# Kernel optimization log

Measured on AMD Instinct MI355X. Metric: run time of the kernel, lower is better.

Reference implementation:

```python
import jax, jax.numpy as jnp
import numpy as np

N_NODES = 100000
N_EDGES = 1600000
NODE_DIM = 64
EDGE_DIM = 32
HIDDEN = 128
OUT_DIM = 64


def setup_inputs() -> dict:
    key = jax.random.key(0)
    ks = jax.random.split(key, 6)
    x = jax.random.normal(ks[0], (N_NODES, NODE_DIM), dtype=jnp.float32)
    edge_attr = jax.random.normal(ks[1], (N_EDGES, EDGE_DIM), dtype=jnp.float32)
    in_dim = 2 * NODE_DIM + EDGE_DIM  # 160
    W1 = jax.random.normal(ks[2], (in_dim, HIDDEN), dtype=jnp.float32) * (1.0 / np.sqrt(in_dim))
    b1 = jnp.zeros((HIDDEN,), dtype=jnp.float32)
    W2 = jax.random.normal(ks[3], (HIDDEN, OUT_DIM), dtype=jnp.float32) * (1.0 / np.sqrt(HIDDEN))
    b2 = jnp.zeros((OUT_DIM,), dtype=jnp.float32)
    edge_index = jax.random.randint(ks[4], (2, N_EDGES), 0, N_NODES, dtype=jnp.int64)
    return {"x": x, "edge_attr": edge_attr, "W1": W1, "b1": b1, "W2": W2, "b2": b2,
            "edge_index": edge_index}


def reference(x, edge_attr, W1, b1, W2, b2, edge_index):
    src, tgt = edge_index[0], edge_index[1]
    # gather source/target node features, concat with edge features: [E, 2*node_dim+edge_dim]
    merged = jnp.concatenate([x[src], x[tgt], edge_attr], axis=1)
    h = jax.nn.relu(merged @ W1 + b1)   # [E, HIDDEN]
    return h @ W2 + b2                  # [E, OUT_DIM]
```

## Files before the change

### kernel.cpp

```cpp
#include <hip/hip_runtime.h>

#define E_TOTAL 1600000
#define N_NODES 100000
#define ND 64
#define ED 32
#define IN_DIM 160
#define HID 128
#define OUTD 64

#define TM 128
#define H_STRIDE 136

typedef short v8s __attribute__((ext_vector_type(8)));
typedef float v4f __attribute__((ext_vector_type(4)));

__device__ __forceinline__ unsigned short f2bf(float f) {
    union { float f; unsigned u; } v; v.f = f;
    unsigned u = v.u;
    u += 0x7FFFu + ((u >> 16) & 1u);
    return (unsigned short)(u >> 16);
}

__device__ __forceinline__ v8s cvt8(float4 f0, float4 f1) {
    v8s r;
    r[0] = (short)f2bf(f0.x); r[1] = (short)f2bf(f0.y);
    r[2] = (short)f2bf(f0.z); r[3] = (short)f2bf(f0.w);
    r[4] = (short)f2bf(f1.x); r[5] = (short)f2bf(f1.y);
    r[6] = (short)f2bf(f1.z); r[7] = (short)f2bf(f1.w);
    return r;
}

__global__ void prep_x(const float* __restrict__ x, unsigned short* __restrict__ xbf) {
    int i = blockIdx.x * blockDim.x + threadIdx.x;
    if (i < N_NODES * ND) xbf[i] = f2bf(x[i]);
}

__global__ void prep_weights(const float* __restrict__ W1, const float* __restrict__ W2,
                             unsigned short* __restrict__ w1f, unsigned short* __restrict__ w2f) {
    int i = blockIdx.x * blockDim.x + threadIdx.x;
    if (i < IN_DIM * HID) {
        int t8 = i & 7, lane = (i >> 3) & 63, jk = i >> 9;
        int kk = jk >> 3, jt = jk & 7, cc = lane & 15, qq = lane >> 4;
        int n = jt * 16 + cc, k = kk * 32 + qq * 8 + t8;
        w1f[i] = f2bf(W1[k * HID + n]);
    } else if (i < IN_DIM * HID + HID * OUTD) {
        int u = i - IN_DIM * HID;
        int t8 = u & 7, lane = (u >> 3) & 63, jk = u >> 9;
        int kk = jk >> 2, jt = jk & 3, cc = lane & 15, qq = lane >> 4;
        int n = jt * 16 + cc, k = kk * 32 + qq * 8 + t8;
        w2f[u] = f2bf(W2[k * OUTD + n]);
    }
}

template<bool XBF>
__global__ __launch_bounds__(256, 4) void edge_mlp(
    const float* __restrict__ x, const unsigned short* __restrict__ xbf,
    const float* __restrict__ ea,
    const float* __restrict__ b1, const float* __restrict__ b2,
    const int* __restrict__ eidx,
    const unsigned short* __restrict__ w1f, const unsigned short* __restrict__ w2f,
    float* __restrict__ out)
{
    __shared__ unsigned short h[TM * H_STRIDE];

    const int tid = threadIdx.x, lane = tid & 63, w = tid >> 6;
    const int wr = w >> 1, wc = w & 1, c = lane & 15, q = lane >> 4;
    const int e0 = blockIdx.x * TM;

    int eRow[4], srcOff[4], tgtOff[4];
#pragma unroll
    for (int i = 0; i < 4; ++i) {
        eRow[i] = e0 + wr * 64 + i * 16 + c;
        srcOff[i] = eidx[eRow[i]] * ND;
        tgtOff[i] = eidx[E_TOTAL + eRow[i]] * ND;
    }

    v4f acc[4][4] = {};
#pragma unroll
    for (int kk = 0; kk < 5; ++kk) {
        v8s a[4];
#pragma unroll
        for (int i = 0; i < 4; ++i) {
            if (kk < 4) {
                const int off = (kk < 2 ? srcOff[i] : tgtOff[i]) + (kk & 1) * 32 + q * 8;
                if (XBF) {
                    a[i] = *(const v8s*)(xbf + off);
                } else {
                    const float4* p = (const float4*)(x + off);
                    a[i] = cvt8(p[0], p[1]);
                }
            } else {
                const float4* p = (const float4*)(ea + (long)eRow[i] * ED + q * 8);
                a[i] = cvt8(p[0], p[1]);
            }
        }
        v8s b[4];
#pragma unroll
        for (int j = 0; j < 4; ++j)
            b[j] = *(const v8s*)(w1f + ((kk * 8 + wc * 4 + j) * 64 + lane) * 8);
#pragma unroll
        for (int i = 0; i < 4; ++i)
#pragma unroll
            for (int j = 0; j < 4; ++j)
                acc[i][j] = __builtin_amdgcn_mfma_f32_16x16x32_bf16(a[i], b[j], acc[i][j], 0, 0, 0);
    }

#pragma unroll
    for (int j = 0; j < 4; ++j) {
        const float bias = b1[wc * 64 + j * 16 + c];
#pragma unroll
        for (int i = 0; i < 4; ++i) {
#pragma unroll
            for (int r = 0; r < 4; ++r) {
                float v = acc[i][j][r] + bias;
                v = v > 0.f ? v : 0.f;
                h[(wr * 64 + i * 16 + q * 4 + r) * H_STRIDE + wc * 64 + j * 16 + c] = f2bf(v);
            }
        }
    }
    __syncthreads();

    v4f acc2[4][2] = {};
#pragma unroll
    for (int kk = 0; kk < 4; ++kk) {
        v8s a[4];
#pragma unroll
        for (int i = 0; i < 4; ++i)
            a[i] = *(const v8s*)(h + (wr * 64 + i * 16 + c) * H_STRIDE + kk * 32 + q * 8);
        v8s b[2];
#pragma unroll
        for (int j = 0; j < 2; ++j)
            b[j] = *(const v8s*)(w2f + ((kk * 4 + wc * 2 + j) * 64 + lane) * 8);
#pragma unroll
        for (int i = 0; i < 4; ++i)
#pragma unroll
            for (int j = 0; j < 2; ++j)
                acc2[i][j] = __builtin_amdgcn_mfma_f32_16x16x32_bf16(a[i], b[j], acc2[i][j], 0, 0, 0);
    }

#pragma unroll
    for (int j = 0; j < 2; ++j) {
        const float bias = b2[wc * 32 + j * 16 + c];
#pragma unroll
        for (int i = 0; i < 4; ++i) {
#pragma unroll
            for (int r = 0; r < 4; ++r) {
                const long e = (long)e0 + wr * 64 + i * 16 + q * 4 + r;
                out[e * OUTD + wc * 32 + j * 16 + c] = acc2[i][j][r] + bias;
            }
        }
    }
}

extern "C" void kernel_launch(void* const* d_in, const int* in_sizes, int n_in,
                              void* d_out, int out_size, void* d_ws, size_t ws_size,
                              hipStream_t stream) {
    const float* x  = (const float*)d_in[0];
    const float* ea = (const float*)d_in[1];
    const float* W1 = (const float*)d_in[2];
    const float* b1 = (const float*)d_in[3];
    const float* W2 = (const float*)d_in[4];
    const float* b2 = (const float*)d_in[5];
    const int* eidx = (const int*)d_in[6];
    float* out = (float*)d_out;

    const size_t nx = (size_t)N_NODES * ND;
    const size_t need = (nx + IN_DIM * HID + HID * OUTD) * 2;
    const int nw = IN_DIM * HID + HID * OUTD;

    if (ws_size >= need) {
        unsigned short* xbf = (unsigned short*)d_ws;
        unsigned short* w1f = xbf + nx;
        unsigned short* w2f = w1f + IN_DIM * HID;
        prep_x<<<(int)((nx + 255) / 256), 256, 0, stream>>>(x, xbf);
        prep_weights<<<(nw + 255) / 256, 256, 0, stream>>>(W1, W2, w1f, w2f);
        edge_mlp<true><<<E_TOTAL / TM, 256, 0, stream>>>(x, xbf, ea, b1, b2, eidx, w1f, w2f, out);
    } else {
        unsigned short* w1f = (unsigned short*)d_ws;
        unsigned short* w2f = w1f + IN_DIM * HID;
        prep_weights<<<(nw + 255) / 256, 256, 0, stream>>>(W1, W2, w1f, w2f);
        edge_mlp<false><<<E_TOTAL / TM, 256, 0, stream>>>(x, nullptr, ea, b1, b2, eidx, w1f, w2f, out);
    }
}
```

Baseline: 734.0 us.

## Process two edge tiles per block with software prefetch of next tile's gathers

Each block now handles two 128-edge tiles. While the second GEMM of the first tile runs, the block prefetches the second tile's node-feature gathers and edge attributes into registers, so gather latency overlaps with MFMA work. Non-temporal loads and stores are used for the streamed edge attributes, indices and output to reduce cache pollution. Launch bounds drop from 4 to 3 blocks per SM to make room for the extra prefetch registers, which lowers occupancy and halves the grid size.

```diff
diff --git a/kernel.cpp b/kernel.cpp
--- a/kernel.cpp
+++ b/kernel.cpp
@@ -21,18 +21,19 @@
     return (unsigned short)(u >> 16);
 }
 
-__device__ __forceinline__ v8s cvt8(float4 f0, float4 f1) {
+__device__ __forceinline__ v8s cvt8v(v4f f0, v4f f1) {
     v8s r;
-    r[0] = (short)f2bf(f0.x); r[1] = (short)f2bf(f0.y);
-    r[2] = (short)f2bf(f0.z); r[3] = (short)f2bf(f0.w);
-    r[4] = (short)f2bf(f1.x); r[5] = (short)f2bf(f1.y);
-    r[6] = (short)f2bf(f1.z); r[7] = (short)f2bf(f1.w);
+#pragma unroll
+    for (int t = 0; t < 4; ++t) {
+        r[t]     = (short)f2bf(f0[t]);
+        r[t + 4] = (short)f2bf(f1[t]);
+    }
     return r;
 }
 
 __global__ void prep_x(const float* __restrict__ x, unsigned short* __restrict__ xbf) {
     int i = blockIdx.x * blockDim.x + threadIdx.x;
-    if (i < N_NODES * ND) xbf[i] = f2bf(x[i]);
+    if (i < N_NODES * ND) xbf[i] = f2bf(__builtin_nontemporal_load(x + i));
 }
 
 __global__ void prep_weights(const float* __restrict__ W1, const float* __restrict__ W2,
@@ -52,8 +53,118 @@
     }
 }
 
+template<bool XBF, bool PREFETCH>
+__device__ __forceinline__ void tile_body(
+    unsigned short* h,
+    const float* __restrict__ x, const unsigned short* __restrict__ xbf,
+    const float* __restrict__ ea,
+    const float* __restrict__ b1, const float* __restrict__ b2,
+    const unsigned short* __restrict__ w1f, const unsigned short* __restrict__ w2f,
+    float* __restrict__ out,
+    const int lane, const int wr, const int wc, const int c, const int q,
+    const int (&eRow)[4], const int (&srcOff)[4], const int (&tgtOff)[4],
+    v8s (&ax)[4][4], v4f (&eaf)[4][2],
+    const int (&eRowN)[4], const int (&srcOffN)[4], const int (&tgtOffN)[4],
+    v8s (&axN)[4][4], v4f (&eafN)[4][2])
+{
+    v4f acc[4][4] = {};
+#pragma unroll
+    for (int kk = 0; kk < 5; ++kk) {
+        v8s a[4];
+#pragma unroll
+        for (int i = 0; i < 4; ++i) {
+            if (kk < 4) {
+                if constexpr (XBF) {
+                    a[i] = ax[i][kk];
+                } else {
+                    const int off = (kk < 2 ? srcOff[i] : tgtOff[i]) + (kk & 1) * 32 + q * 8;
+                    const v4f* p = (const v4f*)(x + off);
+                    a[i] = cvt8v(p[0], p[1]);
+                }
+            } else {
+                a[i] = cvt8v(eaf[i][0], eaf[i][1]);
+            }
+        }
+        v8s b[4];
+#pragma unroll
+        for (int j = 0; j < 4; ++j)
+            b[j] = *(const v8s*)(w1f + ((kk * 8 + wc * 4 + j) * 64 + lane) * 8);
+#pragma unroll
+        for (int i = 0; i < 4; ++i)
+#pragma unroll
+            for (int j = 0; j < 4; ++j)
+                acc[i][j] = __builtin_amdgcn_mfma_f32_16x16x32_bf16(a[i], b[j], acc[i][j], 0, 0, 0);
+    }
+
+#pragma unroll
+    for (int j = 0; j < 4; ++j) {
+        const float bias = b1[wc * 64 + j * 16 + c];
+#pragma unroll
+        for (int i = 0; i < 4; ++i) {
+#pragma unroll
+            for (int r = 0; r < 4; ++r) {
+                float v = acc[i][j][r] + bias;
+                v = v > 0.f ? v : 0.f;
+                h[(wr * 64 + i * 16 + q * 4 + r) * H_STRIDE + wc * 64 + j * 16 + c] = f2bf(v);
+            }
+        }
+    }
+    __syncthreads();
+
+    if constexpr (PREFETCH && XBF) {
+#pragma unroll
+        for (int i = 0; i < 4; ++i) {
+            axN[i][0] = *(const v8s*)(xbf + srcOffN[i] + q * 8);
+            axN[i][1] = *(const v8s*)(xbf + srcOffN[i] + 32 + q * 8);
+            axN[i][2] = *(const v8s*)(xbf + tgtOffN[i] + q * 8);
+            axN[i][3] = *(const v8s*)(xbf + tgtOffN[i] + 32 + q * 8);
+        }
+    }
+
+    v4f acc2[4][2] = {};
+#pragma unroll
+    for (int kk = 0; kk < 4; ++kk) {
+        v8s a[4];
+#pragma unroll
+        for (int i = 0; i < 4; ++i)
+            a[i] = *(const v8s*)(h + (wr * 64 + i * 16 + c) * H_STRIDE + kk * 32 + q * 8);
+        v8s b[2];
+#pragma unroll
+        for (int j = 0; j < 2; ++j)
+            b[j] = *(const v8s*)(w2f + ((kk * 4 + wc * 2 + j) * 64 + lane) * 8);
+#pragma unroll
+        for (int i = 0; i < 4; ++i)
+#pragma unroll
+            for (int j = 0; j < 2; ++j)
+                acc2[i][j] = __builtin_amdgcn_mfma_f32_16x16x32_bf16(a[i], b[j], acc2[i][j], 0, 0, 0);
+    }
+
+    if constexpr (PREFETCH) {
+#pragma unroll
+        for (int i = 0; i < 4; ++i) {
+            const v4f* p = (const v4f*)(ea + (long)eRowN[i] * ED + q * 8);
+            eafN[i][0] = __builtin_nontemporal_load(p);
+            eafN[i][1] = __builtin_nontemporal_load(p + 1);
+        }
+    }
+
+#pragma unroll
+    for (int j = 0; j < 2; ++j) {
+        const float bias = b2[wc * 32 + j * 16 + c];
+#pragma unroll
+        for (int i = 0; i < 4; ++i) {
+#pragma unroll
+            for (int r = 0; r < 4; ++r) {
+                const long e = (long)(eRow[i] - c + q * 4 + r);
+                __builtin_nontemporal_store(acc2[i][j][r] + bias,
+                                            out + e * OUTD + wc * 32 + j * 16 + c);
+            }
+        }
+    }
+}
+
 template<bool XBF>
-__global__ __launch_bounds__(256, 4) void edge_mlp(
+__global__ __launch_bounds__(256, 3) void edge_mlp(
     const float* __restrict__ x, const unsigned short* __restrict__ xbf,
     const float* __restrict__ ea,
     const float* __restrict__ b1, const float* __restrict__ b2,
@@ -65,91 +176,45 @@
 
     const int tid = threadIdx.x, lane = tid & 63, w = tid >> 6;
     const int wr = w >> 1, wc = w & 1, c = lane & 15, q = lane >> 4;
-    const int e0 = blockIdx.x * TM;
-
-    int eRow[4], srcOff[4], tgtOff[4];
+    const int e0 = blockIdx.x * (2 * TM);
+
+    int eRowA[4], srcOffA[4], tgtOffA[4], eRowB[4], srcOffB[4], tgtOffB[4];
 #pragma unroll
     for (int i = 0; i < 4; ++i) {
-        eRow[i] = e0 + wr * 64 + i * 16 + c;
-        srcOff[i] = eidx[eRow[i]] * ND;
-        tgtOff[i] = eidx[E_TOTAL + eRow[i]] * ND;
-    }
-
-    v4f acc[4][4] = {};
-#pragma unroll
-    for (int kk = 0; kk < 5; ++kk) {
-        v8s a[4];
-#pragma unroll
-        for (int i = 0; i < 4; ++i) {
-            if (kk < 4) {
-                const int off = (kk < 2 ? srcOff[i] : tgtOff[i]) + (kk & 1) * 32 + q * 8;
-                if (XBF) {
-                    a[i] = *(const v8s*)(xbf + off);
-                } else {
-                    const float4* p = (const float4*)(x + off);
-                    a[i] = cvt8(p[0], p[1]);
-                }
-            } else {
-                const float4* p = (const float4*)(ea + (long)eRow[i] * ED + q * 8);
-                a[i] = cvt8(p[0], p[1]);
-            }
-        }
-        v8s b[4];
-#pragma unroll
-        for (int j = 0; j < 4; ++j)
-            b[j] = *(const v8s*)(w1f + ((kk * 8 + wc * 4 + j) * 64 + lane) * 8);
-#pragma unroll
-        for (int i = 0; i < 4; ++i)
-#pragma unroll
-            for (int j = 0; j < 4; ++j)
-                acc[i][j] = __builtin_amdgcn_mfma_f32_16x16x32_bf16(a[i], b[j], acc[i][j], 0, 0, 0);
-    }
-
-#pragma unroll
-    for (int j = 0; j < 4; ++j) {
-        const float bias = b1[wc * 64 + j * 16 + c];
-#pragma unroll
-        for (int i = 0; i < 4; ++i) {
-#pragma unroll
-            for (int r = 0; r < 4; ++r) {
-                float v = acc[i][j][r] + bias;
-                v = v > 0.f ? v : 0.f;
-                h[(wr * 64 + i * 16 + q * 4 + r) * H_STRIDE + wc * 64 + j * 16 + c] = f2bf(v);
-            }
-        }
-    }
+        eRowA[i] = e0 + wr * 64 + i * 16 + c;
+        eRowB[i] = eRowA[i] + TM;
+        srcOffA[i] = __builtin_nontemporal_load(eidx + eRowA[i]) * ND;
+        tgtOffA[i] = __builtin_nontemporal_load(eidx + E_TOTAL + eRowA[i]) * ND;
+        srcOffB[i] = __builtin_nontemporal_load(eidx + eRowB[i]) * ND;
+        tgtOffB[i] = __builtin_nontemporal_load(eidx + E_TOTAL + eRowB[i]) * ND;
+    }
+
+    v8s axA[4][4], axB[4][4];
+    v4f eafA[4][2], eafB[4][2];
+
+    if constexpr (XBF) {
+#pragma unroll
+        for (int i = 0; i < 4; ++i) {
+            axA[i][0] = *(const v8s*)(xbf + srcOffA[i] + q * 8);
+            axA[i][1] = *(const v8s*)(xbf + srcOffA[i] + 32 + q * 8);
+            axA[i][2] = *(const v8s*)(xbf + tgtOffA[i] + q * 8);
+            axA[i][3] = *(const v8s*)(xbf + tgtOffA[i] + 32 + q * 8);
+        }
+    }
+#pragma unroll
+    for (int i = 0; i < 4; ++i) {
+        const v4f* p = (const v4f*)(ea + (long)eRowA[i] * ED + q * 8);
+        eafA[i][0] = __builtin_nontemporal_load(p);
+        eafA[i][1] = __builtin_nontemporal_load(p + 1);
+    }
+
+    tile_body<XBF, true>(h, x, xbf, ea, b1, b2, w1f, w2f, out, lane, wr, wc, c, q,
+                         eRowA, srcOffA, tgtOffA, axA, eafA,
+                         eRowB, srcOffB, tgtOffB, axB, eafB);
     __syncthreads();
-
-    v4f acc2[4][2] = {};
-#pragma unroll
-    for (int kk = 0; kk < 4; ++kk) {
-        v8s a[4];
-#pragma unroll
-        for (int i = 0; i < 4; ++i)
-            a[i] = *(const v8s*)(h + (wr * 64 + i * 16 + c) * H_STRIDE + kk * 32 + q * 8);
-        v8s b[2];
-#pragma unroll
-        for (int j = 0; j < 2; ++j)
-            b[j] = *(const v8s*)(w2f + ((kk * 4 + wc * 2 + j) * 64 + lane) * 8);
-#pragma unroll
-        for (int i = 0; i < 4; ++i)
-#pragma unroll
-            for (int j = 0; j < 2; ++j)
-                acc2[i][j] = __builtin_amdgcn_mfma_f32_16x16x32_bf16(a[i], b[j], acc2[i][j], 0, 0, 0);
-    }
-
-#pragma unroll
-    for (int j = 0; j < 2; ++j) {
-        const float bias = b2[wc * 32 + j * 16 + c];
-#pragma unroll
-        for (int i = 0; i < 4; ++i) {
-#pragma unroll
-            for (int r = 0; r < 4; ++r) {
-                const long e = (long)e0 + wr * 64 + i * 16 + q * 4 + r;
-                out[e * OUTD + wc * 32 + j * 16 + c] = acc2[i][j][r] + bias;
-            }
-        }
-    }
+    tile_body<XBF, false>(h, x, xbf, ea, b1, b2, w1f, w2f, out, lane, wr, wc, c, q,
+                          eRowB, srcOffB, tgtOffB, axB, eafB,
+                          eRowB, srcOffB, tgtOffB, axB, eafB);
 }
 
 extern "C" void kernel_launch(void* const* d_in, const int* in_sizes, int n_in,
@@ -167,6 +232,7 @@
     const size_t nx = (size_t)N_NODES * ND;
     const size_t need = (nx + IN_DIM * HID + HID * OUTD) * 2;
     const int nw = IN_DIM * HID + HID * OUTD;
+    const int grid = E_TOTAL / (2 * TM);
 
     if (ws_size >= need) {
         unsigned short* xbf = (unsigned short*)d_ws;
@@ -174,11 +240,11 @@
         unsigned short* w2f = w1f + IN_DIM * HID;
         prep_x<<<(int)((nx + 255) / 256), 256, 0, stream>>>(x, xbf);
         prep_weights<<<(nw + 255) / 256, 256, 0, stream>>>(W1, W2, w1f, w2f);
-        edge_mlp<true><<<E_TOTAL / TM, 256, 0, stream>>>(x, xbf, ea, b1, b2, eidx, w1f, w2f, out);
+        edge_mlp<true><<<grid, 256, 0, stream>>>(x, xbf, ea, b1, b2, eidx, w1f, w2f, out);
     } else {
         unsigned short* w1f = (unsigned short*)d_ws;
         unsigned short* w2f = w1f + IN_DIM * HID;
         prep_weights<<<(nw + 255) / 256, 256, 0, stream>>>(W1, W2, w1f, w2f);
-        edge_mlp<false><<<E_TOTAL / TM, 256, 0, stream>>>(x, nullptr, ea, b1, b2, eidx, w1f, w2f, out);
-    }
-}
+        edge_mlp<false><<<grid, 256, 0, stream>>>(x, nullptr, ea, b1, b2, eidx, w1f, w2f, out);
+    }
+}
```

New measurement: 839.9 us. 1.14x slower.
